# Kernel tuning notes

Measured on AMD Instinct MI355X. Metric: run time of the kernel, lower is better.

Reference implementation:

```python
import jax, jax.numpy as jnp
import numpy as np

N_NODES = 10000
N_EDGES = 100000
C = 64          # in_channels == out_channels (required by x_i + x_m)
D_EDGE = 16     # edge_attr feature dim


def setup_inputs() -> dict:
    key = jax.random.key(0)
    k_x, k_ei, k_ea, k_w, k_b, k_r, k_bias = jax.random.split(key, 7)
    x = jax.random.normal(k_x, (N_NODES, C), dtype=jnp.float32)
    edge_index = jax.random.randint(k_ei, (2, N_EDGES), 0, N_NODES, dtype=jnp.int32)
    edge_attr = jax.random.normal(k_ea, (N_EDGES, D_EDGE), dtype=jnp.float32)
    # nn = Linear(D_EDGE -> C*C), producing per-edge [C, C] weight matrices
    W_nn = jax.random.normal(k_w, (D_EDGE, C * C), dtype=jnp.float32) * (1.0 / np.sqrt(D_EDGE))
    b_nn = jax.random.normal(k_b, (C * C,), dtype=jnp.float32) * 0.01
    root = jax.random.normal(k_r, (C, C), dtype=jnp.float32) * (1.0 / np.sqrt(C))
    bias = jax.random.normal(k_bias, (C,), dtype=jnp.float32) * 0.01
    return {"x": x, "edge_index": edge_index, "edge_attr": edge_attr,
            "W_nn": W_nn, "b_nn": b_nn, "root": root, "bias": bias}


def reference(x, edge_index, edge_attr, W_nn, b_nn, root, bias):
    N, Cc = x.shape
    row, col = edge_index[0], edge_index[1]
    # per-edge weight matrices from nn(edge_attr): [E, C, C]
    e = (edge_attr @ W_nn + b_nn).reshape(-1, Cc, Cc)
    # gather source features and apply edge-conditioned matmul: [E, C]
    m = jnp.einsum('ec,eco->eo', x[row], e)
    # Faithful to torch loop: x_m[i] = m[col == i].mean() -> SCALAR mean over
    # all elements of incoming messages, broadcast across the feature row.
    seg_sum = jax.ops.segment_sum(m.sum(axis=1), col, num_segments=N)       # [N]
    cnt = jax.ops.segment_sum(jnp.ones_like(col, dtype=x.dtype), col,
                              num_segments=N) * Cc                            # [N]
    mean = jnp.where(cnt > 0, seg_sum / jnp.maximum(cnt, 1.0), 0.0)          # [N]
    x_m = jnp.broadcast_to(mean[:, None], (N, Cc))                            # [N, C]
    # root transform + bias
    out = x @ root + bias + x_m
    return out
```

## Files before the change

kernel.cpp:

```cpp
#include <hip/hip_runtime.h>
#include <hip/hip_bf16.h>


#define CC 64
#define DE 16

__global__ __launch_bounds__(1024) void k_wsum(const float* __restrict__ W,
                                               const float* __restrict__ b,
                                               float* __restrict__ wsum,
                                               float* __restrict__ bsum) {
    int p = threadIdx.x;
    int d = p >> 6, c = p & 63;
    const float4* w4 = (const float4*)(W + (size_t)d * (CC * CC) + c * CC);
    float s = 0.f;
#pragma unroll
    for (int i = 0; i < 16; ++i) { float4 v = w4[i]; s += v.x + v.y + v.z + v.w; }
    wsum[p] = s;
    if (p < CC) {
        const float4* b4 = (const float4*)(b + p * CC);
        float sb = 0.f;
#pragma unroll
        for (int i = 0; i < 16; ++i) { float4 v = b4[i]; sb += v.x + v.y + v.z + v.w; }
        bsum[p] = sb;
    }
}

__global__ __launch_bounds__(256) void k_node(const float* __restrict__ x,
                                              const float* __restrict__ wsum_bsum,
                                              float* __restrict__ g,
                                              float* __restrict__ h,
                                              int N) {
    __shared__ float ws[1024 + 64];
    int tid = threadIdx.x;
#pragma unroll
    for (int i = 0; i < 4; ++i) ws[tid + i * 256] = wsum_bsum[tid + i * 256];
    if (tid < 64) ws[1024 + tid] = wsum_bsum[1024 + tid];
    __syncthreads();

    int n = blockIdx.x * 256 + tid;
    if (n >= N) return;

    const float4* x4 = (const float4*)(x + (size_t)n * CC);
    const float4* ws4 = (const float4*)ws;
    const float4* bs4 = (const float4*)(ws + 1024);

    float acc[DE];
#pragma unroll
    for (int d = 0; d < DE; ++d) acc[d] = 0.f;
    float hh = 0.f;

#pragma unroll
    for (int c4 = 0; c4 < 16; ++c4) {
        float4 xv = x4[c4];
        float4 bv = bs4[c4];
        hh += bv.x * xv.x + bv.y * xv.y + bv.z * xv.z + bv.w * xv.w;
#pragma unroll
        for (int d = 0; d < DE; ++d) {
            float4 wv = ws4[d * 16 + c4];
            acc[d] += wv.x * xv.x + wv.y * xv.y + wv.z * xv.z + wv.w * xv.w;
        }
    }
    float4* g4 = (float4*)(g + (size_t)n * DE);
    g4[0] = make_float4(acc[0], acc[1], acc[2], acc[3]);
    g4[1] = make_float4(acc[4], acc[5], acc[6], acc[7]);
    g4[2] = make_float4(acc[8], acc[9], acc[10], acc[11]);
    g4[3] = make_float4(acc[12], acc[13], acc[14], acc[15]);
    h[n] = hh;
}

__global__ __launch_bounds__(256) void k_edge(const int* __restrict__ ei,
                                              const float* __restrict__ ea,
                                              const float* __restrict__ g,
                                              const float* __restrict__ h,
                                              float* __restrict__ seg,
                                              float* __restrict__ cnt,
                                              int E) {
    int e = blockIdx.x * 256 + threadIdx.x;
    if (e >= E) return;
    int r = ei[e];
    int cn = ei[E + e];
    const float4* a4 = (const float4*)(ea + (size_t)e * DE);
    const float4* g4 = (const float4*)(g + (size_t)r * DE);
    float4 a0 = a4[0], a1 = a4[1], a2 = a4[2], a3 = a4[3];
    float4 g0 = g4[0], g1 = g4[1], g2 = g4[2], g3 = g4[3];
    float s = h[r]
        + a0.x * g0.x + a0.y * g0.y + a0.z * g0.z + a0.w * g0.w
        + a1.x * g1.x + a1.y * g1.y + a1.z * g1.z + a1.w * g1.w
        + a2.x * g2.x + a2.y * g2.y + a2.z * g2.z + a2.w * g2.w
        + a3.x * g3.x + a3.y * g3.y + a3.z * g3.z + a3.w * g3.w;
    atomicAdd(seg + cn, s);
    atomicAdd(cnt + cn, 1.0f);
}

__global__ __launch_bounds__(256) void k_final(const float* __restrict__ x,
                                               const float* __restrict__ root,
                                               const float* __restrict__ bias,
                                               const float* __restrict__ seg,
                                               const float* __restrict__ cnt,
                                               float* __restrict__ out,
                                               int N) {
    __shared__ float rt[CC * CC];
    __shared__ float xs[4 * CC];
    __shared__ float bi[CC];
    __shared__ float mn[4];
    int tid = threadIdx.x;
    int n0 = blockIdx.x * 4;

#pragma unroll
    for (int i = 0; i < 16; ++i) rt[tid + i * 256] = root[tid + i * 256];
    if (n0 * CC + tid < N * CC) xs[tid] = x[(size_t)n0 * CC + tid];
    if (tid < CC) bi[tid] = bias[tid];
    if (tid < 4 && n0 + tid < N) {
        float c = cnt[n0 + tid];
        mn[tid] = c > 0.f ? seg[n0 + tid] / (c * (float)CC) : 0.f;
    }
    __syncthreads();

    int nl = tid >> 6, c = tid & 63;
    int n = n0 + nl;
    if (n >= N) return;
    float acc = bi[c] + mn[nl];
#pragma unroll
    for (int k = 0; k < CC; ++k) acc += xs[nl * CC + k] * rt[k * CC + c];
    out[(size_t)n * CC + c] = acc;
}

extern "C" void kernel_launch(void* const* d_in, const int* in_sizes, int n_in,
                              void* d_out, int out_size, void* d_ws, size_t ws_size,
                              hipStream_t stream) {
    const float* x    = (const float*)d_in[0];
    const int*   ei   = (const int*)  d_in[1];
    const float* ea   = (const float*)d_in[2];
    const float* W    = (const float*)d_in[3];
    const float* b    = (const float*)d_in[4];
    const float* root = (const float*)d_in[5];
    const float* bias = (const float*)d_in[6];
    float* out = (float*)d_out;
    float* ws  = (float*)d_ws;

    const int N = in_sizes[0] / CC;
    const int E = in_sizes[1] / 2;

    float* wsum = ws;
    float* h    = ws + 1088;
    float* seg  = ws + 1088 + N;
    float* cnt  = ws + 1088 + 2 * N;
    float* g    = ws + 1088 + 3 * N;

    hipMemsetAsync(seg, 0, (size_t)2 * N * sizeof(float), stream);

    k_wsum<<<1, 1024, 0, stream>>>(W, b, wsum, wsum + 1024);
    k_node<<<(N + 255) / 256, 256, 0, stream>>>(x, wsum, g, h, N);
    k_edge<<<(E + 255) / 256, 256, 0, stream>>>(ei, ea, g, h, seg, cnt, E);
    k_final<<<(N + 3) / 4, 256, 0, stream>>>(x, root, bias, seg, cnt, out, N);
}
```

Measured before the change: 113.5 us.

## Fold memset into parallel prep kernel and retile node and final kernels

Replaces the separate memset and the single-block weight-sum kernel with one multi-block prep kernel. It zeroes the segment and count buffers and computes the weight row sums with wave shuffles. k_node now uses 64-thread blocks that read the summed weights directly from global memory instead of staging them in LDS, and it preloads each node's x row into registers. k_final handles 16 nodes per block with padded LDS for x and float4 outputs, so the root matrix is loaded fewer times. Together these cut a launch and raise parallelism, at the cost of weight reads in k_node going through cache rather than LDS.

```diff
diff --git a/kernel.cpp b/kernel.cpp
--- a/kernel.cpp
+++ b/kernel.cpp
@@ -4,45 +4,42 @@
 
 #define CC 64
 #define DE 16
+#define PAD 65
 
-__global__ __launch_bounds__(1024) void k_wsum(const float* __restrict__ W,
-                                               const float* __restrict__ b,
-                                               float* __restrict__ wsum,
-                                               float* __restrict__ bsum) {
-    int p = threadIdx.x;
-    int d = p >> 6, c = p & 63;
-    const float4* w4 = (const float4*)(W + (size_t)d * (CC * CC) + c * CC);
-    float s = 0.f;
+__global__ __launch_bounds__(256) void k_prep(const float* __restrict__ W,
+                                              const float* __restrict__ b,
+                                              float* __restrict__ wsum,
+                                              float* __restrict__ zreg,
+                                              int zcount, int total_waves) {
+    int gtid = blockIdx.x * 256 + threadIdx.x;
+    for (int i = gtid; i < zcount; i += gridDim.x * 256) zreg[i] = 0.f;
+
+    int lane = threadIdx.x & 63;
+    int wid  = gtid >> 6;
+    for (int p = wid; p < 1024 + CC; p += total_waves) {
+        float v = (p < 1024) ? W[(size_t)p * CC + lane]
+                             : b[(size_t)(p - 1024) * CC + lane];
 #pragma unroll
-    for (int i = 0; i < 16; ++i) { float4 v = w4[i]; s += v.x + v.y + v.z + v.w; }
-    wsum[p] = s;
-    if (p < CC) {
-        const float4* b4 = (const float4*)(b + p * CC);
-        float sb = 0.f;
-#pragma unroll
-        for (int i = 0; i < 16; ++i) { float4 v = b4[i]; sb += v.x + v.y + v.z + v.w; }
-        bsum[p] = sb;
+        for (int off = 32; off; off >>= 1) v += __shfl_xor(v, off, 64);
+        if (lane == 0) wsum[p] = v;
     }
 }
 
-__global__ __launch_bounds__(256) void k_node(const float* __restrict__ x,
-                                              const float* __restrict__ wsum_bsum,
-                                              float* __restrict__ g,
-                                              float* __restrict__ h,
-                                              int N) {
-    __shared__ float ws[1024 + 64];
-    int tid = threadIdx.x;
-#pragma unroll
-    for (int i = 0; i < 4; ++i) ws[tid + i * 256] = wsum_bsum[tid + i * 256];
-    if (tid < 64) ws[1024 + tid] = wsum_bsum[1024 + tid];
-    __syncthreads();
-
-    int n = blockIdx.x * 256 + tid;
+__global__ __launch_bounds__(64) void k_node(const float* __restrict__ x,
+                                             const float* __restrict__ wb,
+                                             float* __restrict__ g,
+                                             float* __restrict__ h,
+                                             int N) {
+    int n = blockIdx.x * 64 + threadIdx.x;
     if (n >= N) return;
 
-    const float4* x4 = (const float4*)(x + (size_t)n * CC);
-    const float4* ws4 = (const float4*)ws;
-    const float4* bs4 = (const float4*)(ws + 1024);
+    const float4* x4  = (const float4*)(x + (size_t)n * CC);
+    const float4* ws4 = (const float4*)wb;
+    const float4* bs4 = (const float4*)(wb + 1024);
+
+    float4 xr[16];
+#pragma unroll
+    for (int i = 0; i < 16; ++i) xr[i] = x4[i];
 
     float acc[DE];
 #pragma unroll
@@ -51,7 +48,7 @@
 
 #pragma unroll
     for (int c4 = 0; c4 < 16; ++c4) {
-        float4 xv = x4[c4];
+        float4 xv = xr[c4];
         float4 bv = bs4[c4];
         hh += bv.x * xv.x + bv.y * xv.y + bv.z * xv.z + bv.w * xv.w;
 #pragma unroll
@@ -77,7 +74,7 @@
                                               int E) {
     int e = blockIdx.x * 256 + threadIdx.x;
     if (e >= E) return;
-    int r = ei[e];
+    int r  = ei[e];
     int cn = ei[E + e];
     const float4* a4 = (const float4*)(ea + (size_t)e * DE);
     const float4* g4 = (const float4*)(g + (size_t)r * DE);
@@ -100,29 +97,43 @@
                                                float* __restrict__ out,
                                                int N) {
     __shared__ float rt[CC * CC];
-    __shared__ float xs[4 * CC];
+    __shared__ float xs[16 * PAD];
     __shared__ float bi[CC];
-    __shared__ float mn[4];
+    __shared__ float mn[16];
     int tid = threadIdx.x;
-    int n0 = blockIdx.x * 4;
+    int n0 = blockIdx.x * 16;
 
 #pragma unroll
     for (int i = 0; i < 16; ++i) rt[tid + i * 256] = root[tid + i * 256];
-    if (n0 * CC + tid < N * CC) xs[tid] = x[(size_t)n0 * CC + tid];
+#pragma unroll
+    for (int it = 0; it < 4; ++it) {
+        int i = it * 256 + tid;
+        if ((size_t)n0 * CC + i < (size_t)N * CC)
+            xs[(i >> 6) * PAD + (i & 63)] = x[(size_t)n0 * CC + i];
+    }
     if (tid < CC) bi[tid] = bias[tid];
-    if (tid < 4 && n0 + tid < N) {
+    if (tid < 16 && n0 + tid < N) {
         float c = cnt[n0 + tid];
         mn[tid] = c > 0.f ? seg[n0 + tid] / (c * (float)CC) : 0.f;
     }
     __syncthreads();
 
-    int nl = tid >> 6, c = tid & 63;
+    int nl = tid >> 4, ci = tid & 15;
     int n = n0 + nl;
     if (n >= N) return;
-    float acc = bi[c] + mn[nl];
+
+    const float4* rt4 = (const float4*)rt;
+    const float4* bi4 = (const float4*)bi;
+    float m = mn[nl];
+    float4 bv = bi4[ci];
+    float4 acc = make_float4(bv.x + m, bv.y + m, bv.z + m, bv.w + m);
 #pragma unroll
-    for (int k = 0; k < CC; ++k) acc += xs[nl * CC + k] * rt[k * CC + c];
-    out[(size_t)n * CC + c] = acc;
+    for (int k = 0; k < CC; ++k) {
+        float a  = xs[nl * PAD + k];
+        float4 w = rt4[k * 16 + ci];
+        acc.x += a * w.x; acc.y += a * w.y; acc.z += a * w.z; acc.w += a * w.w;
+    }
+    *(float4*)(out + (size_t)n * CC + ci * 4) = acc;
 }
 
 extern "C" void kernel_launch(void* const* d_in, const int* in_sizes, int n_in,
@@ -147,10 +158,13 @@
     float* cnt  = ws + 1088 + 2 * N;
     float* g    = ws + 1088 + 3 * N;
 
-    hipMemsetAsync(seg, 0, (size_t)2 * N * sizeof(float), stream);
+    int zBlocks = (2 * N + 255) / 256;
+    int nBlocks = (N + 63) / 64;
+    int eBlocks = (E + 255) / 256;
+    int fBlocks = (N + 15) / 16;
 
-    k_wsum<<<1, 1024, 0, stream>>>(W, b, wsum, wsum + 1024);
-    k_node<<<(N + 255) / 256, 256, 0, stream>>>(x, wsum, g, h, N);
-    k_edge<<<(E + 255) / 256, 256, 0, stream>>>(ei, ea, g, h, seg, cnt, E);
-    k_final<<<(N + 3) / 4, 256, 0, stream>>>(x, root, bias, seg, cnt, out, N);
+    k_prep <<<zBlocks, 256, 0, stream>>>(W, b, wsum, seg, 2 * N, zBlocks * 4);
+    k_node <<<nBlocks,  64, 0, stream>>>(x, wsum, g, h, N);
+    k_edge <<<eBlocks, 256, 0, stream>>>(ei, ea, g, h, seg, cnt, E);
+    k_final<<<fBlocks, 256, 0, stream>>>(x, root, bias, seg, cnt, out, N);
 }
```

New measurement: 114.0 us. Within noise of the previous version (+0.5%).
